# Kernel tuning notes

Measured on AMD Instinct MI355X. Metric: run time of the kernel, lower is better.

Reference implementation:

```python
import jax, jax.numpy as jnp
import numpy as np

GROUP_SIZE = 64
SHARED_EXPERT_WEIGHT = 1.0
# FP4 E2M1 codebook: sign bit + {0,.5,1,1.5,2,3,4,6}
FP4_TABLE = jnp.array([0.0, 0.5, 1.0, 1.5, 2.0, 3.0, 4.0, 6.0,
                       -0.0, -0.5, -1.0, -1.5, -2.0, -3.0, -4.0, -6.0], dtype=jnp.float32)


def dequant_fp4(packed, scales, group_size=GROUP_SIZE):
    """packed: [..., K//8, N] int32 (8 nibbles along K per word),
    scales: [..., K//group_size, N] -> dequantized [..., K, N] fp32."""
    shifts = (jnp.arange(8, dtype=jnp.int32) * 4)[:, None]          # [8,1]
    nib = jnp.right_shift(packed[..., :, None, :], shifts) & 0xF     # [..., K//8, 8, N]
    w = FP4_TABLE[nib]
    K = packed.shape[-2] * 8
    w = w.reshape(packed.shape[:-2] + (K, packed.shape[-1]))         # [..., K, N]
    s = jnp.repeat(scales, group_size, axis=-2)                      # [..., K, N]
    return w * s


def setup_inputs() -> dict:
    key = jax.random.key(0)
    ks = jax.random.split(key, 12)
    T, K, I, E, TOPK = 2048, 2048, 1024, 8, 2
    GS = GROUP_SIZE
    MAXI = 2**31 - 1
    u = lambda k, shp: jax.random.uniform(k, shp, jnp.float32, 0.005, 0.02)
    probs = jax.random.uniform(ks[10], (T, TOPK), jnp.float32)
    probs = probs / probs.sum(-1, keepdims=True)
    return {
        "hidden_states": jax.random.normal(ks[0], (T, K), jnp.float32),
        "gate_up_weight_packed": jax.random.randint(ks[1], (E, K // 8, 2 * I), 0, MAXI, jnp.int32),
        "gate_up_scales": u(ks[2], (E, K // GS, 2 * I)),
        "down_weight_packed": jax.random.randint(ks[3], (E, I // 8, K), 0, MAXI, jnp.int32),
        "down_scales": u(ks[4], (E, I // GS, K)),
        "shared_gate_up_packed": jax.random.randint(ks[5], (K // 8, 2 * I), 0, MAXI, jnp.int32),
        "shared_gate_up_scales": u(ks[6], (K // GS, 2 * I)),
        "shared_down_packed": jax.random.randint(ks[7], (I // 8, K), 0, MAXI, jnp.int32),
        "shared_down_scales": u(ks[8], (I // GS, K)),
        "expert_ids": jax.random.randint(ks[9], (T, TOPK), 0, E, jnp.int32),
        "expert_probs": probs,
    }


def reference(hidden_states, gate_up_weight_packed, gate_up_scales,
              down_weight_packed, down_scales,
              shared_gate_up_packed, shared_gate_up_scales,
              shared_down_packed, shared_down_scales,
              expert_ids, expert_probs):
    x = hidden_states                                                # [T, K]
    E = gate_up_weight_packed.shape[0]
    # --- routed experts: dequant + grouped GEMM over all tokens per expert ---
    Wgu = dequant_fp4(gate_up_weight_packed, gate_up_scales)         # [E, K, 2I]
    Wd = dequant_fp4(down_weight_packed, down_scales)                # [E, I, K]
    h = jnp.einsum('tk,ekn->etn', x, Wgu)                            # [E, T, 2I]
    gate, up = jnp.split(h, 2, axis=-1)
    act = jax.nn.silu(gate) * up                                     # [E, T, I]
    y = jnp.einsum('eti,eik->etk', act, Wd)                          # [E, T, K]
    # combine[t,e] = sum over top-k slots routed to e of prob
    one_hot = jax.nn.one_hot(expert_ids, E, dtype=x.dtype)           # [T, topk, E]
    combine = jnp.einsum('tk,tke->te', expert_probs, one_hot)        # [T, E]
    out = jnp.einsum('te,etk->tk', combine, y)                       # [T, K]
    # --- shared expert (always applied, weighted) ---
    Wgu_s = dequant_fp4(shared_gate_up_packed, shared_gate_up_scales)  # [K, 2I]
    Wd_s = dequant_fp4(shared_down_packed, shared_down_scales)         # [I, K]
    hs = x @ Wgu_s
    gs, us = jnp.split(hs, 2, axis=-1)
    shared_out = (jax.nn.silu(gs) * us) @ Wd_s
    return out + SHARED_EXPERT_WEIGHT * shared_out
```

## Files before the change

### kernel.cpp

```cpp
#include <hip/hip_runtime.h>
#include <hip/hip_bf16.h>

#define T_TOK 2048
#define K_DIM 2048
#define I_DIM 1024
#define NE    8
#define TOPK  2
#define GS    64

#define NSLOT  (T_TOK * TOPK)
#define TOTROW (NSLOT + T_TOK)
#define MAXITEM 32

typedef __attribute__((ext_vector_type(8))) short short8;
typedef __attribute__((ext_vector_type(4))) float f32x4;

#define WS_XB   ((size_t)65536)
#define WS_ACT  (WS_XB  + (size_t)2048 * 2048 * 2)
#define WS_Y    (WS_ACT + (size_t)TOTROW * 1024 * 2)


__device__ __forceinline__ unsigned pack2(float a, float b) {
    __hip_bfloat162 h = __float22bfloat162_rn(make_float2(a, b));
    return *reinterpret_cast<unsigned*>(&h);
}

__device__ __forceinline__ unsigned scale2(unsigned p, float s) {
    float f0 = __uint_as_float(p << 16) * s;
    float f1 = __uint_as_float(p & 0xFFFF0000u) * s;
    return pack2(f0, f1);
}

__device__ __forceinline__ float bf2f(ushort h) {
    return __uint_as_float((unsigned)h << 16);
}

__device__ __forceinline__ void dq_word(unsigned w, float s, unsigned o[4]) {
    unsigned lo  = w & 0x0F0F0F0Fu;
    unsigned hi  = (w >> 4) & 0x0F0F0F0Fu;
    unsigned mlo = lo & 0x07070707u, mhi = hi & 0x07070707u;
    unsigned Hlo = __builtin_amdgcn_perm(0x40404040u, 0x3F3F3F00u, mlo);
    unsigned Hhi = __builtin_amdgcn_perm(0x40404040u, 0x3F3F3F00u, mhi);
    unsigned Llo = __builtin_amdgcn_perm(0xC0804000u, 0xC0800000u, mlo);
    unsigned Lhi = __builtin_amdgcn_perm(0xC0804000u, 0xC0800000u, mhi);
    Hlo |= (lo & 0x08080808u) << 4;
    Hhi |= (hi & 0x08080808u) << 4;
    unsigned e01 = __builtin_amdgcn_perm(Hlo, Llo, 0x05010400u);
    unsigned e23 = __builtin_amdgcn_perm(Hlo, Llo, 0x07030602u);
    unsigned o01 = __builtin_amdgcn_perm(Hhi, Lhi, 0x05010400u);
    unsigned o23 = __builtin_amdgcn_perm(Hhi, Lhi, 0x07030602u);
    o[0] = scale2(e01, s); o[1] = scale2(e23, s);
    o[2] = scale2(o01, s); o[3] = scale2(o23, s);
}

__device__ __forceinline__ void gld16(const void* g, void* l) {
    __builtin_amdgcn_global_load_lds(
        (const __attribute__((address_space(1))) unsigned*)g,
        (__attribute__((address_space(3))) unsigned*)l, 16, 0, 0);
}

#define PREP_BLK 2048
#define FRONT_GRID (PREP_BLK + 1)

__global__ __launch_bounds__(256) void k_front(
        const float* __restrict__ x, ushort* __restrict__ xb,
        const int* __restrict__ eids,
        int* __restrict__ gcnt, int* __restrict__ gbase,
        int* __restrict__ tileCnt, int* __restrict__ tileE, int* __restrict__ tileM,
        int* __restrict__ tok, int* __restrict__ inv) {
    int id = blockIdx.x;
    int tid = threadIdx.x;

    if (id < PREP_BLK) {
        int idx = id * 256 + tid;
        const float4* p = (const float4*)(x + (size_t)idx * 8);
        float4 f0 = p[0], f1 = p[1];
        unsigned u0 = pack2(f0.x, f0.z);
        unsigned u1 = pack2(f1.x, f1.z);
        unsigned u2 = pack2(f0.y, f0.w);
        unsigned u3 = pack2(f1.y, f1.w);
        *(int4*)(xb + (size_t)idx * 8) = make_int4(u0, u1, u2, u3);
    } else {
        __shared__ int lcnt[NE], lbase[NE], lcur[NE];
        if (tid < NE) lcnt[tid] = 0;
        __syncthreads();
        for (int i = tid; i < NSLOT; i += 256)
            atomicAdd(&lcnt[eids[i]], 1);
        __syncthreads();
        if (tid == 0) {
            int acc = 0;
            for (int e = 0; e < NE; e++) { lbase[e] = acc; acc += lcnt[e]; }
        }
        __syncthreads();
        if (tid < NE) lcur[tid] = lbase[tid];
        __syncthreads();
        for (int i = tid; i < NSLOT; i += 256) {
            int e = eids[i];
            int pos = atomicAdd(&lcur[e], 1);
            tok[pos] = i >> 1;
            inv[i] = pos;
        }
        for (int t = tid; t < T_TOK; t += 256)
            tok[NSLOT + t] = t;
        if (tid < NE) { gcnt[tid] = lcnt[tid]; gbase[tid] = lbase[tid]; }
        if (tid == 0) {
            gcnt[NE] = T_TOK; gbase[NE] = NSLOT;
            int nt = 0;
            for (int e = 0; e < NE + 1; e++) {
                int c = (e < NE) ? lcnt[e] : T_TOK;
                for (int m = 0; m < c; m += 256) { tileE[nt] = e; tileM[nt] = m; nt++; }
            }
            *tileCnt = nt;
            for (int i = nt; i < 64; i++) { tileE[i] = 0; tileM[i] = 0; }
        }
    }
}

__global__ __launch_bounds__(512) void k_gemm_gateup(
        const ushort* __restrict__ xb,
        const int* __restrict__ gup, const float* __restrict__ gus,
        const int* __restrict__ sup, const float* __restrict__ sus,
        const int* __restrict__ gcnt, const int* __restrict__ gbase,
        const int* __restrict__ tileCnt, const int* __restrict__ tileE,
        const int* __restrict__ tileM,
        const int* __restrict__ tokid, ushort* __restrict__ act) {
    int item = blockIdx.y;
    if (item >= *tileCnt) return;
    int tid = threadIdx.x;
    int e = tileE[item], m0 = tileM[item];
    int cnt = gcnt[e], base = gbase[e];
    int n0 = blockIdx.x * 64;
    const int* wp; const float* sc;
    if (e < NE) { wp = gup + (size_t)e * 256 * 2048; sc = gus + (size_t)e * 32 * 2048; }
    else        { wp = sup; sc = sus; }

    __shared__ __align__(16) ushort xs[2][256 * 64];
    __shared__ __align__(16) ushort bs[128 * 64];

    int lane = tid & 63, wv = tid >> 6;
    int lid = lane & 15, quad = lane >> 4;
    int wr = wv >> 1, wc = wv & 1;
    int l8 = lane >> 3, l7 = lane & 7;
    int chunk = (l7 ^ l8) * 8;

    const ushort* aSrc[4];
    #pragma unroll
    for (int it = 0; it < 4; it++) {
        int rA = wv * 32 + it * 8 + l8;
        int t = (m0 + rA < cnt) ? tokid[base + m0 + rA] : 0;
        aSrc[it] = xb + (size_t)t * K_DIM + chunk;
    }

    int nloc = tid & 127;
    int kw0 = (tid >> 7) * 2;
    int bj = nloc & 63, bh = nloc >> 6;
    int ncol = (bj < 32) ? (n0 + bh * 32 + bj) : (I_DIM + n0 + bh * 32 + (bj - 32));
    int bd0 = nloc * 64 + ((kw0    ) ^ (nloc & 7)) * 8;
    int bd1 = nloc * 64 + ((kw0 + 1) ^ (nloc & 7)) * 8;

    const int NT = K_DIM / 64;
    const int* wq = wp + (size_t)kw0 * 2048 + ncol;
    const float* sq = sc + ncol;

    #pragma unroll
    for (int it = 0; it < 4; it++) {
        gld16(aSrc[it], &xs[0][(wv * 4 + it) * 512]);
        aSrc[it] += 64;
    }
    unsigned w0 = (unsigned)wq[0];
    unsigned w1 = (unsigned)wq[2048];
    float s = *sq;
    wq += 16384; sq += 2048;

    f32x4 acc[4][4] = {};
    int pp = 0;

    for (int t = 0; t < NT; ++t) {
        __syncthreads();
        {
            unsigned o[4];
            dq_word(w0, s, o); *(int4*)&bs[bd0] = make_int4(o[0], o[1], o[2], o[3]);
            dq_word(w1, s, o); *(int4*)&bs[bd1] = make_int4(o[0], o[1], o[2], o[3]);
        }
        __syncthreads();
        if (t + 1 < NT) {
            #pragma unroll
            for (int it = 0; it < 4; it++) {
                gld16(aSrc[it], &xs[pp ^ 1][(wv * 4 + it) * 512]);
                aSrc[it] += 64;
            }
            w0 = (unsigned)wq[0];
            w1 = (unsigned)wq[2048];
            s = *sq;
            wq += 16384; sq += 2048;
        }
        __builtin_amdgcn_sched_barrier(0);
        __builtin_amdgcn_s_setprio(1);
        #pragma unroll
        for (int ks = 0; ks < 2; ks++) {
            int slot = ((ks * 4 + quad) ^ l7) * 8;
            short8 a[4], b[4];
            #pragma unroll
            for (int mt = 0; mt < 4; mt++)
                a[mt] = *(const short8*)&xs[pp][(wr * 64 + mt * 16 + lid) * 64 + slot];
            #pragma unroll
            for (int nt = 0; nt < 4; nt++)
                b[nt] = *(const short8*)&bs[(wc * 64 + nt * 16 + lid) * 64 + slot];
            #pragma unroll
            for (int mt = 0; mt < 4; mt++)
                #pragma unroll
                for (int nt = 0; nt < 4; nt++)
                    acc[mt][nt] = __builtin_amdgcn_mfma_f32_16x16x32_bf16(
                        a[mt], b[nt], acc[mt][nt], 0, 0, 0);
        }
        __builtin_amdgcn_s_setprio(0);
        pp ^= 1;
    }

    int c7 = lid & 7;
    int delta = ((c7 >> 1) + ((c7 & 1) << 2)) - c7;
    #pragma unroll
    for (int mt = 0; mt < 4; mt++) {
        #pragma unroll
        for (int i = 0; i < 4; i++) {
            int row = wr * 64 + mt * 16 + quad * 4 + i;
            if (m0 + row < cnt) {
                size_t p = (size_t)(base + m0 + row);
                #pragma unroll
                for (int nt = 0; nt < 2; nt++) {
                    float g = acc[mt][nt][i], u = acc[mt][nt + 2][i];
                    float vv = g / (1.f + __expf(-g)) * u;
                    int ncol2 = n0 + wc * 32 + nt * 16 + lid;
                    __hip_bfloat16 hb = __float2bfloat16(vv);
                    act[p * I_DIM + ncol2 + delta] = *reinterpret_cast<ushort*>(&hb);
                }
            }
        }
    }
}

__global__ __launch_bounds__(512) void k_gemm_down(
        const ushort* __restrict__ actb,
        const int* __restrict__ dwp, const float* __restrict__ dsc,
        const int* __restrict__ sdp, const float* __restrict__ sds,
        const int* __restrict__ gcnt, const int* __restrict__ gbase,
        const int* __restrict__ tileCnt, const int* __restrict__ tileE,
        const int* __restrict__ tileM,
        ushort* __restrict__ y) {
    int item = blockIdx.y;
    if (item >= *tileCnt) return;
    int tid = threadIdx.x;
    int e = tileE[item], m0 = tileM[item];
    int cnt = gcnt[e], base = gbase[e];
    int n0 = blockIdx.x * 128;
    const int* wp; const float* sc;
    if (e < NE) { wp = dwp + (size_t)e * 128 * 2048; sc = dsc + (size_t)e * 16 * 2048; }
    else        { wp = sdp; sc = sds; }

    __shared__ __align__(16) ushort xs[2][256 * 64];
    __shared__ __align__(16) ushort bs[128 * 64];

    int lane = tid & 63, wv = tid >> 6;
    int lid = lane & 15, quad = lane >> 4;
    int wr = wv >> 1, wc = wv & 1;
    int l8 = lane >> 3, l7 = lane & 7;
    int chunk = (l7 ^ l8) * 8;

    const ushort* aSrc[4];
    #pragma unroll
    for (int it = 0; it < 4; it++) {
        int rA = wv * 32 + it * 8 + l8;
        int rr = m0 + rA; if (rr >= cnt) rr = cnt - 1;
        aSrc[it] = actb + (size_t)(base + rr) * I_DIM + chunk;
    }

    int nloc = tid & 127;
    int kw0 = (tid >> 7) * 2;
    int ncol = n0 + nloc;
    int bd0 = nloc * 64 + ((kw0    ) ^ (nloc & 7)) * 8;
    int bd1 = nloc * 64 + ((kw0 + 1) ^ (nloc & 7)) * 8;

    const int NT = I_DIM / 64;
    const int* wq = wp + (size_t)kw0 * 2048 + ncol;
    const float* sq = sc + ncol;

    #pragma unroll
    for (int it = 0; it < 4; it++) {
        gld16(aSrc[it], &xs[0][(wv * 4 + it) * 512]);
        aSrc[it] += 64;
    }
    unsigned w0 = (unsigned)wq[0];
    unsigned w1 = (unsigned)wq[2048];
    float s = *sq;
    wq += 16384; sq += 2048;

    f32x4 acc[4][4] = {};
    int pp = 0;

    for (int t = 0; t < NT; ++t) {
        __syncthreads();
        {
            unsigned o[4];
            dq_word(w0, s, o); *(int4*)&bs[bd0] = make_int4(o[0], o[1], o[2], o[3]);
            dq_word(w1, s, o); *(int4*)&bs[bd1] = make_int4(o[0], o[1], o[2], o[3]);
        }
        __syncthreads();
        if (t + 1 < NT) {
            #pragma unroll
            for (int it = 0; it < 4; it++) {
                gld16(aSrc[it], &xs[pp ^ 1][(wv * 4 + it) * 512]);
                aSrc[it] += 64;
            }
            w0 = (unsigned)wq[0];
            w1 = (unsigned)wq[2048];
            s = *sq;
            wq += 16384; sq += 2048;
        }
        __builtin_amdgcn_sched_barrier(0);
        __builtin_amdgcn_s_setprio(1);
        #pragma unroll
        for (int ks = 0; ks < 2; ks++) {
            int slot = ((ks * 4 + quad) ^ l7) * 8;
            short8 a[4], b[4];
            #pragma unroll
            for (int mt = 0; mt < 4; mt++)
                a[mt] = *(const short8*)&xs[pp][(wr * 64 + mt * 16 + lid) * 64 + slot];
            #pragma unroll
            for (int nt = 0; nt < 4; nt++)
                b[nt] = *(const short8*)&bs[(wc * 64 + nt * 16 + lid) * 64 + slot];
            #pragma unroll
            for (int mt = 0; mt < 4; mt++)
                #pragma unroll
                for (int nt = 0; nt < 4; nt++)
                    acc[mt][nt] = __builtin_amdgcn_mfma_f32_16x16x32_bf16(
                        a[mt], b[nt], acc[mt][nt], 0, 0, 0);
        }
        __builtin_amdgcn_s_setprio(0);
        pp ^= 1;
    }

    #pragma unroll
    for (int mt = 0; mt < 4; mt++) {
        #pragma unroll
        for (int i = 0; i < 4; i++) {
            int row = wr * 64 + mt * 16 + quad * 4 + i;
            if (m0 + row < cnt) {
                ushort* yrow = y + (size_t)(base + m0 + row) * 2048 + n0 + wc * 64 + lid;
                #pragma unroll
                for (int nt = 0; nt < 4; nt++) {
                    __hip_bfloat16 hb = __float2bfloat16(acc[mt][nt][i]);
                    yrow[nt * 16] = *reinterpret_cast<ushort*>(&hb);
                }
            }
        }
    }
}

__global__ __launch_bounds__(256) void k_combine(
        const ushort* __restrict__ y, const int* __restrict__ inv,
        const float* __restrict__ prb, float* __restrict__ out) {
    int idx = blockIdx.x * 256 + threadIdx.x;
    int t = idx >> 8;
    int c = (idx & 255) * 8;
    int p0 = inv[2 * t], p1 = inv[2 * t + 1];
    float w0 = prb[2 * t], w1 = prb[2 * t + 1];
    int4 a = *(const int4*)(y + (size_t)p0 * 2048 + c);
    int4 b = *(const int4*)(y + (size_t)p1 * 2048 + c);
    int4 s = *(const int4*)(y + (size_t)(NSLOT + t) * 2048 + c);
    const ushort* au = (const ushort*)&a;
    const ushort* bu = (const ushort*)&b;
    const ushort* su = (const ushort*)&s;
    float o[8];
    #pragma unroll
    for (int j = 0; j < 8; j++)
        o[j] = w0 * bf2f(au[j]) + w1 * bf2f(bu[j]) + bf2f(su[j]);
    *(float4*)(out + (size_t)t * 2048 + c)     = *(float4*)&o[0];
    *(float4*)(out + (size_t)t * 2048 + c + 4) = *(float4*)&o[4];
}

extern "C" void kernel_launch(void* const* d_in, const int* in_sizes, int n_in,
                              void* d_out, int out_size, void* d_ws, size_t ws_size,
                              hipStream_t stream) {
    const float* x    = (const float*)d_in[0];
    const int*   gup  = (const int*)d_in[1];
    const float* gus  = (const float*)d_in[2];
    const int*   dwp  = (const int*)d_in[3];
    const float* dsc  = (const float*)d_in[4];
    const int*   sup  = (const int*)d_in[5];
    const float* sus  = (const float*)d_in[6];
    const int*   sdp  = (const int*)d_in[7];
    const float* sds  = (const float*)d_in[8];
    const int*   eids = (const int*)d_in[9];
    const float* prb  = (const float*)d_in[10];
    float* out = (float*)d_out;

    char*   ws      = (char*)d_ws;
    int*    gcnt    = (int*)(ws + 0);
    int*    gbase   = (int*)(ws + 64);
    int*    tileCnt = (int*)(ws + 128);
    int*    tileE   = (int*)(ws + 192);
    int*    tileM   = (int*)(ws + 448);
    int*    tok     = (int*)(ws + 1024);
    int*    inv     = (int*)(ws + 25600);
    ushort* xb      = (ushort*)(ws + WS_XB);
    ushort* act     = (ushort*)(ws + WS_ACT);
    ushort* y       = (ushort*)(ws + WS_Y);

    k_front<<<FRONT_GRID, 256, 0, stream>>>(
        x, xb, eids, gcnt, gbase, tileCnt, tileE, tileM, tok, inv);
    k_gemm_gateup<<<dim3(I_DIM / 64, MAXITEM), 512, 0, stream>>>(
        xb, gup, gus, sup, sus, gcnt, gbase, tileCnt, tileE, tileM, tok, act);
    k_gemm_down<<<dim3(K_DIM / 128, MAXITEM), 512, 0, stream>>>(
        act, dwp, dsc, sdp, sds, gcnt, gbase, tileCnt, tileE, tileM, y);
    k_combine<<<(T_TOK * K_DIM / 8) / 256, 256, 0, stream>>>(y, inv, prb, out);
}
```

Baseline: 234.2 us.

## Double-buffer dequantized weights and widen GEMM tiles with interleaved phase pipeline

Both grouped GEMMs move to 256x256 output tiles (8 waves as 2x4), so each block covers twice as many N columns, and the dequantized B tile gets double-buffered in LDS. The K loop is split into four MFMA phases. Between phases the code interleaves the next A-tile async loads, the dequantization of the next B sub-slice and weight prefetch two steps ahead, using explicit s_barrier and waitcnt control. The aim is to hide the global-load and dequant latency behind MFMA and to raise the per-block reuse of A. The cost is more LDS (about 128KB), twice the accumulator registers, fewer blocks in the grid, and fragile hand-tuned waitcnt ordering.

```diff
diff --git a/kernel.cpp b/kernel.cpp
--- a/kernel.cpp
+++ b/kernel.cpp
@@ -116,7 +116,7 @@
     }
 }
 
-__global__ __launch_bounds__(512) void k_gemm_gateup(
+__global__ __launch_bounds__(512, 2) void k_gemm_gateup(
         const ushort* __restrict__ xb,
         const int* __restrict__ gup, const float* __restrict__ gus,
         const int* __restrict__ sup, const float* __restrict__ sus,
@@ -129,17 +129,17 @@
     int tid = threadIdx.x;
     int e = tileE[item], m0 = tileM[item];
     int cnt = gcnt[e], base = gbase[e];
-    int n0 = blockIdx.x * 64;
+    int n0 = blockIdx.x * 128;
     const int* wp; const float* sc;
     if (e < NE) { wp = gup + (size_t)e * 256 * 2048; sc = gus + (size_t)e * 32 * 2048; }
     else        { wp = sup; sc = sus; }
 
     __shared__ __align__(16) ushort xs[2][256 * 64];
-    __shared__ __align__(16) ushort bs[128 * 64];
+    __shared__ __align__(16) ushort bs[2][256 * 64];
 
     int lane = tid & 63, wv = tid >> 6;
     int lid = lane & 15, quad = lane >> 4;
-    int wr = wv >> 1, wc = wv & 1;
+    int wr = wv >> 2, wc = wv & 3;
     int l8 = lane >> 3, l7 = lane & 7;
     int chunk = (l7 ^ l8) * 8;
 
@@ -151,95 +151,176 @@
         aSrc[it] = xb + (size_t)t * K_DIM + chunk;
     }
 
-    int nloc = tid & 127;
-    int kw0 = (tid >> 7) * 2;
-    int bj = nloc & 63, bh = nloc >> 6;
-    int ncol = (bj < 32) ? (n0 + bh * 32 + bj) : (I_DIM + n0 + bh * 32 + (bj - 32));
-    int bd0 = nloc * 64 + ((kw0    ) ^ (nloc & 7)) * 8;
-    int bd1 = nloc * 64 + ((kw0 + 1) ^ (nloc & 7)) * 8;
+    int col = tid & 255;
+    int kw0 = (tid >> 8) * 4;
+    int jj = col & 63, wq_ = col >> 6;
+    int ncol = (jj < 32) ? (n0 + wq_ * 32 + jj) : (I_DIM + n0 + wq_ * 32 + (jj - 32));
+    int bd0 = col * 64 + ((kw0    ) ^ (col & 7)) * 8;
+    int bd1 = col * 64 + ((kw0 + 1) ^ (col & 7)) * 8;
+    int bd2 = col * 64 + ((kw0 + 2) ^ (col & 7)) * 8;
+    int bd3 = col * 64 + ((kw0 + 3) ^ (col & 7)) * 8;
 
     const int NT = K_DIM / 64;
-    const int* wq = wp + (size_t)kw0 * 2048 + ncol;
-    const float* sq = sc + ncol;
 
     #pragma unroll
     for (int it = 0; it < 4; it++) {
         gld16(aSrc[it], &xs[0][(wv * 4 + it) * 512]);
         aSrc[it] += 64;
     }
-    unsigned w0 = (unsigned)wq[0];
-    unsigned w1 = (unsigned)wq[2048];
-    float s = *sq;
-    wq += 16384; sq += 2048;
-
-    f32x4 acc[4][4] = {};
-    int pp = 0;
-
+    {
+        float s0 = sc[ncol];
+        unsigned o[4];
+        unsigned w;
+        w = (unsigned)wp[(size_t)(kw0    ) * 2048 + ncol];
+        dq_word(w, s0, o); *(int4*)&bs[0][bd0] = make_int4(o[0], o[1], o[2], o[3]);
+        w = (unsigned)wp[(size_t)(kw0 + 1) * 2048 + ncol];
+        dq_word(w, s0, o); *(int4*)&bs[0][bd1] = make_int4(o[0], o[1], o[2], o[3]);
+        w = (unsigned)wp[(size_t)(kw0 + 2) * 2048 + ncol];
+        dq_word(w, s0, o); *(int4*)&bs[0][bd2] = make_int4(o[0], o[1], o[2], o[3]);
+        w = (unsigned)wp[(size_t)(kw0 + 3) * 2048 + ncol];
+        dq_word(w, s0, o); *(int4*)&bs[0][bd3] = make_int4(o[0], o[1], o[2], o[3]);
+    }
+    unsigned wd0 = (unsigned)wp[(size_t)(8 + kw0    ) * 2048 + ncol];
+    unsigned wd1 = (unsigned)wp[(size_t)(8 + kw0 + 1) * 2048 + ncol];
+    unsigned wd2 = (unsigned)wp[(size_t)(8 + kw0 + 2) * 2048 + ncol];
+    unsigned wd3 = (unsigned)wp[(size_t)(8 + kw0 + 3) * 2048 + ncol];
+    float sd = sc[2048 + ncol];
+    __syncthreads();
+
+    f32x4 acc[8][4] = {};
+
+    #pragma unroll 1
     for (int t = 0; t < NT; ++t) {
-        __syncthreads();
-        {
-            unsigned o[4];
-            dq_word(w0, s, o); *(int4*)&bs[bd0] = make_int4(o[0], o[1], o[2], o[3]);
-            dq_word(w1, s, o); *(int4*)&bs[bd1] = make_int4(o[0], o[1], o[2], o[3]);
-        }
-        __syncthreads();
-        if (t + 1 < NT) {
-            #pragma unroll
-            for (int it = 0; it < 4; it++) {
-                gld16(aSrc[it], &xs[pp ^ 1][(wv * 4 + it) * 512]);
-                aSrc[it] += 64;
-            }
-            w0 = (unsigned)wq[0];
-            w1 = (unsigned)wq[2048];
-            s = *sq;
-            wq += 16384; sq += 2048;
-        }
-        __builtin_amdgcn_sched_barrier(0);
-        __builtin_amdgcn_s_setprio(1);
-        #pragma unroll
-        for (int ks = 0; ks < 2; ks++) {
-            int slot = ((ks * 4 + quad) ^ l7) * 8;
-            short8 a[4], b[4];
-            #pragma unroll
-            for (int mt = 0; mt < 4; mt++)
-                a[mt] = *(const short8*)&xs[pp][(wr * 64 + mt * 16 + lid) * 64 + slot];
-            #pragma unroll
-            for (int nt = 0; nt < 4; nt++)
-                b[nt] = *(const short8*)&bs[(wc * 64 + nt * 16 + lid) * 64 + slot];
-            #pragma unroll
-            for (int mt = 0; mt < 4; mt++)
-                #pragma unroll
-                for (int nt = 0; nt < 4; nt++)
-                    acc[mt][nt] = __builtin_amdgcn_mfma_f32_16x16x32_bf16(
-                        a[mt], b[nt], acc[mt][nt], 0, 0, 0);
-        }
-        __builtin_amdgcn_s_setprio(0);
-        pp ^= 1;
+        int p = t & 1, q = p ^ 1;
+        int t2 = (t + 2 < NT) ? (t + 2) : (NT - 1);
+        const int* wlp = wp + (size_t)(t2 * 8 + kw0) * 2048 + ncol;
+        unsigned wl0, wl1, wl2, wl3; float sl;
+        short8 a[4], b[4];
+        unsigned o[4];
+
+        {
+            int slot = (quad ^ l7) * 8;
+            #pragma unroll
+            for (int mt = 0; mt < 4; mt++)
+                a[mt] = *(const short8*)&xs[p][(wr * 128 + mt * 16 + lid) * 64 + slot];
+            #pragma unroll
+            for (int nt = 0; nt < 4; nt++)
+                b[nt] = *(const short8*)&bs[p][(wc * 64 + nt * 16 + lid) * 64 + slot];
+        }
+        gld16(aSrc[0], &xs[q][(wv * 4 + 0) * 512]); aSrc[0] += 64;
+        gld16(aSrc[1], &xs[q][(wv * 4 + 1) * 512]); aSrc[1] += 64;
+        dq_word(wd0, sd, o); *(int4*)&bs[q][bd0] = make_int4(o[0], o[1], o[2], o[3]);
+        __builtin_amdgcn_s_barrier();
+        asm volatile("s_waitcnt lgkmcnt(0)" ::: "memory");
+        __builtin_amdgcn_sched_barrier(0);
+        __builtin_amdgcn_s_setprio(1);
+        #pragma unroll
+        for (int mt = 0; mt < 4; mt++)
+            #pragma unroll
+            for (int nt = 0; nt < 4; nt++)
+                acc[mt][nt] = __builtin_amdgcn_mfma_f32_16x16x32_bf16(
+                    a[mt], b[nt], acc[mt][nt], 0, 0, 0);
+        __builtin_amdgcn_s_setprio(0);
+        __builtin_amdgcn_s_barrier();
+
+        {
+            int slot = (quad ^ l7) * 8;
+            #pragma unroll
+            for (int mt = 0; mt < 4; mt++)
+                a[mt] = *(const short8*)&xs[p][(wr * 128 + 64 + mt * 16 + lid) * 64 + slot];
+        }
+        gld16(aSrc[2], &xs[q][(wv * 4 + 2) * 512]); aSrc[2] += 64;
+        gld16(aSrc[3], &xs[q][(wv * 4 + 3) * 512]); aSrc[3] += 64;
+        dq_word(wd1, sd, o); *(int4*)&bs[q][bd1] = make_int4(o[0], o[1], o[2], o[3]);
+        __builtin_amdgcn_s_barrier();
+        asm volatile("s_waitcnt lgkmcnt(0)" ::: "memory");
+        __builtin_amdgcn_sched_barrier(0);
+        __builtin_amdgcn_s_setprio(1);
+        #pragma unroll
+        for (int mt = 0; mt < 4; mt++)
+            #pragma unroll
+            for (int nt = 0; nt < 4; nt++)
+                acc[4 + mt][nt] = __builtin_amdgcn_mfma_f32_16x16x32_bf16(
+                    a[mt], b[nt], acc[4 + mt][nt], 0, 0, 0);
+        __builtin_amdgcn_s_setprio(0);
+        __builtin_amdgcn_s_barrier();
+
+        {
+            int slot = ((4 + quad) ^ l7) * 8;
+            #pragma unroll
+            for (int mt = 0; mt < 4; mt++)
+                a[mt] = *(const short8*)&xs[p][(wr * 128 + mt * 16 + lid) * 64 + slot];
+            #pragma unroll
+            for (int nt = 0; nt < 4; nt++)
+                b[nt] = *(const short8*)&bs[p][(wc * 64 + nt * 16 + lid) * 64 + slot];
+        }
+        wl0 = (unsigned)wlp[0];
+        wl1 = (unsigned)wlp[2048];
+        dq_word(wd2, sd, o); *(int4*)&bs[q][bd2] = make_int4(o[0], o[1], o[2], o[3]);
+        __builtin_amdgcn_s_barrier();
+        asm volatile("s_waitcnt lgkmcnt(0)" ::: "memory");
+        __builtin_amdgcn_sched_barrier(0);
+        __builtin_amdgcn_s_setprio(1);
+        #pragma unroll
+        for (int mt = 0; mt < 4; mt++)
+            #pragma unroll
+            for (int nt = 0; nt < 4; nt++)
+                acc[mt][nt] = __builtin_amdgcn_mfma_f32_16x16x32_bf16(
+                    a[mt], b[nt], acc[mt][nt], 0, 0, 0);
+        __builtin_amdgcn_s_setprio(0);
+        __builtin_amdgcn_s_barrier();
+
+        {
+            int slot = ((4 + quad) ^ l7) * 8;
+            #pragma unroll
+            for (int mt = 0; mt < 4; mt++)
+                a[mt] = *(const short8*)&xs[p][(wr * 128 + 64 + mt * 16 + lid) * 64 + slot];
+        }
+        wl2 = (unsigned)wlp[4096];
+        wl3 = (unsigned)wlp[6144];
+        sl  = sc[(size_t)t2 * 2048 + ncol];
+        dq_word(wd3, sd, o); *(int4*)&bs[q][bd3] = make_int4(o[0], o[1], o[2], o[3]);
+        __builtin_amdgcn_s_barrier();
+        asm volatile("s_waitcnt lgkmcnt(0)" ::: "memory");
+        __builtin_amdgcn_sched_barrier(0);
+        __builtin_amdgcn_s_setprio(1);
+        #pragma unroll
+        for (int mt = 0; mt < 4; mt++)
+            #pragma unroll
+            for (int nt = 0; nt < 4; nt++)
+                acc[4 + mt][nt] = __builtin_amdgcn_mfma_f32_16x16x32_bf16(
+                    a[mt], b[nt], acc[4 + mt][nt], 0, 0, 0);
+        __builtin_amdgcn_s_setprio(0);
+        asm volatile("s_waitcnt vmcnt(5)" ::: "memory");
+        __builtin_amdgcn_s_barrier();
+        __builtin_amdgcn_sched_barrier(0);
+
+        wd0 = wl0; wd1 = wl1; wd2 = wl2; wd3 = wl3; sd = sl;
     }
 
     int c7 = lid & 7;
     int delta = ((c7 >> 1) + ((c7 & 1) << 2)) - c7;
     #pragma unroll
-    for (int mt = 0; mt < 4; mt++) {
+    for (int am = 0; am < 8; am++) {
         #pragma unroll
         for (int i = 0; i < 4; i++) {
-            int row = wr * 64 + mt * 16 + quad * 4 + i;
+            int row = wr * 128 + am * 16 + quad * 4 + i;
             if (m0 + row < cnt) {
-                size_t p = (size_t)(base + m0 + row);
+                size_t pr = (size_t)(base + m0 + row);
                 #pragma unroll
                 for (int nt = 0; nt < 2; nt++) {
-                    float g = acc[mt][nt][i], u = acc[mt][nt + 2][i];
+                    float g = acc[am][nt][i], u = acc[am][nt + 2][i];
                     float vv = g / (1.f + __expf(-g)) * u;
                     int ncol2 = n0 + wc * 32 + nt * 16 + lid;
                     __hip_bfloat16 hb = __float2bfloat16(vv);
-                    act[p * I_DIM + ncol2 + delta] = *reinterpret_cast<ushort*>(&hb);
+                    act[pr * I_DIM + ncol2 + delta] = *reinterpret_cast<ushort*>(&hb);
                 }
             }
         }
     }
 }
 
-__global__ __launch_bounds__(512) void k_gemm_down(
+__global__ __launch_bounds__(512, 2) void k_gemm_down(
         const ushort* __restrict__ actb,
         const int* __restrict__ dwp, const float* __restrict__ dsc,
         const int* __restrict__ sdp, const float* __restrict__ sds,
@@ -252,17 +333,17 @@
     int tid = threadIdx.x;
     int e = tileE[item], m0 = tileM[item];
     int cnt = gcnt[e], base = gbase[e];
-    int n0 = blockIdx.x * 128;
+    int n0 = blockIdx.x * 256;
     const int* wp; const float* sc;
     if (e < NE) { wp = dwp + (size_t)e * 128 * 2048; sc = dsc + (size_t)e * 16 * 2048; }
     else        { wp = sdp; sc = sds; }
 
     __shared__ __align__(16) ushort xs[2][256 * 64];
-    __shared__ __align__(16) ushort bs[128 * 64];
+    __shared__ __align__(16) ushort bs[2][256 * 64];
 
     int lane = tid & 63, wv = tid >> 6;
     int lid = lane & 15, quad = lane >> 4;
-    int wr = wv >> 1, wc = wv & 1;
+    int wr = wv >> 2, wc = wv & 3;
     int l8 = lane >> 3, l7 = lane & 7;
     int chunk = (l7 ^ l8) * 8;
 
@@ -274,81 +355,162 @@
         aSrc[it] = actb + (size_t)(base + rr) * I_DIM + chunk;
     }
 
-    int nloc = tid & 127;
-    int kw0 = (tid >> 7) * 2;
-    int ncol = n0 + nloc;
-    int bd0 = nloc * 64 + ((kw0    ) ^ (nloc & 7)) * 8;
-    int bd1 = nloc * 64 + ((kw0 + 1) ^ (nloc & 7)) * 8;
+    int col = tid & 255;
+    int kw0 = (tid >> 8) * 4;
+    int ncol = n0 + col;
+    int bd0 = col * 64 + ((kw0    ) ^ (col & 7)) * 8;
+    int bd1 = col * 64 + ((kw0 + 1) ^ (col & 7)) * 8;
+    int bd2 = col * 64 + ((kw0 + 2) ^ (col & 7)) * 8;
+    int bd3 = col * 64 + ((kw0 + 3) ^ (col & 7)) * 8;
 
     const int NT = I_DIM / 64;
-    const int* wq = wp + (size_t)kw0 * 2048 + ncol;
-    const float* sq = sc + ncol;
 
     #pragma unroll
     for (int it = 0; it < 4; it++) {
         gld16(aSrc[it], &xs[0][(wv * 4 + it) * 512]);
         aSrc[it] += 64;
     }
-    unsigned w0 = (unsigned)wq[0];
-    unsigned w1 = (unsigned)wq[2048];
-    float s = *sq;
-    wq += 16384; sq += 2048;
-
-    f32x4 acc[4][4] = {};
-    int pp = 0;
-
+    {
+        float s0 = sc[ncol];
+        unsigned o[4];
+        unsigned w;
+        w = (unsigned)wp[(size_t)(kw0    ) * 2048 + ncol];
+        dq_word(w, s0, o); *(int4*)&bs[0][bd0] = make_int4(o[0], o[1], o[2], o[3]);
+        w = (unsigned)wp[(size_t)(kw0 + 1) * 2048 + ncol];
+        dq_word(w, s0, o); *(int4*)&bs[0][bd1] = make_int4(o[0], o[1], o[2], o[3]);
+        w = (unsigned)wp[(size_t)(kw0 + 2) * 2048 + ncol];
+        dq_word(w, s0, o); *(int4*)&bs[0][bd2] = make_int4(o[0], o[1], o[2], o[3]);
+        w = (unsigned)wp[(size_t)(kw0 + 3) * 2048 + ncol];
+        dq_word(w, s0, o); *(int4*)&bs[0][bd3] = make_int4(o[0], o[1], o[2], o[3]);
+    }
+    unsigned wd0 = (unsigned)wp[(size_t)(8 + kw0    ) * 2048 + ncol];
+    unsigned wd1 = (unsigned)wp[(size_t)(8 + kw0 + 1) * 2048 + ncol];
+    unsigned wd2 = (unsigned)wp[(size_t)(8 + kw0 + 2) * 2048 + ncol];
+    unsigned wd3 = (unsigned)wp[(size_t)(8 + kw0 + 3) * 2048 + ncol];
+    float sd = sc[2048 + ncol];
+    __syncthreads();
+
+    f32x4 acc[8][4] = {};
+
+    #pragma unroll 1
     for (int t = 0; t < NT; ++t) {
-        __syncthreads();
-        {
-            unsigned o[4];
-            dq_word(w0, s, o); *(int4*)&bs[bd0] = make_int4(o[0], o[1], o[2], o[3]);
-            dq_word(w1, s, o); *(int4*)&bs[bd1] = make_int4(o[0], o[1], o[2], o[3]);
-        }
-        __syncthreads();
-        if (t + 1 < NT) {
-            #pragma unroll
-            for (int it = 0; it < 4; it++) {
-                gld16(aSrc[it], &xs[pp ^ 1][(wv * 4 + it) * 512]);
-                aSrc[it] += 64;
-            }
-            w0 = (unsigned)wq[0];
-            w1 = (unsigned)wq[2048];
-            s = *sq;
-            wq += 16384; sq += 2048;
-        }
-        __builtin_amdgcn_sched_barrier(0);
-        __builtin_amdgcn_s_setprio(1);
-        #pragma unroll
-        for (int ks = 0; ks < 2; ks++) {
-            int slot = ((ks * 4 + quad) ^ l7) * 8;
-            short8 a[4], b[4];
-            #pragma unroll
-            for (int mt = 0; mt < 4; mt++)
-                a[mt] = *(const short8*)&xs[pp][(wr * 64 + mt * 16 + lid) * 64 + slot];
-            #pragma unroll
-            for (int nt = 0; nt < 4; nt++)
-                b[nt] = *(const short8*)&bs[(wc * 64 + nt * 16 + lid) * 64 + slot];
-            #pragma unroll
-            for (int mt = 0; mt < 4; mt++)
-                #pragma unroll
-                for (int nt = 0; nt < 4; nt++)
-                    acc[mt][nt] = __builtin_amdgcn_mfma_f32_16x16x32_bf16(
-                        a[mt], b[nt], acc[mt][nt], 0, 0, 0);
-        }
-        __builtin_amdgcn_s_setprio(0);
-        pp ^= 1;
-    }
-
-    #pragma unroll
-    for (int mt = 0; mt < 4; mt++) {
+        int p = t & 1, q = p ^ 1;
+        int t2 = (t + 2 < NT) ? (t + 2) : (NT - 1);
+        const int* wlp = wp + (size_t)(t2 * 8 + kw0) * 2048 + ncol;
+        unsigned wl0, wl1, wl2, wl3; float sl;
+        short8 a[4], b[4];
+        unsigned o[4];
+
+        {
+            int slot = (quad ^ l7) * 8;
+            #pragma unroll
+            for (int mt = 0; mt < 4; mt++)
+                a[mt] = *(const short8*)&xs[p][(wr * 128 + mt * 16 + lid) * 64 + slot];
+            #pragma unroll
+            for (int nt = 0; nt < 4; nt++)
+                b[nt] = *(const short8*)&bs[p][(wc * 64 + nt * 16 + lid) * 64 + slot];
+        }
+        gld16(aSrc[0], &xs[q][(wv * 4 + 0) * 512]); aSrc[0] += 64;
+        gld16(aSrc[1], &xs[q][(wv * 4 + 1) * 512]); aSrc[1] += 64;
+        dq_word(wd0, sd, o); *(int4*)&bs[q][bd0] = make_int4(o[0], o[1], o[2], o[3]);
+        __builtin_amdgcn_s_barrier();
+        asm volatile("s_waitcnt lgkmcnt(0)" ::: "memory");
+        __builtin_amdgcn_sched_barrier(0);
+        __builtin_amdgcn_s_setprio(1);
+        #pragma unroll
+        for (int mt = 0; mt < 4; mt++)
+            #pragma unroll
+            for (int nt = 0; nt < 4; nt++)
+                acc[mt][nt] = __builtin_amdgcn_mfma_f32_16x16x32_bf16(
+                    a[mt], b[nt], acc[mt][nt], 0, 0, 0);
+        __builtin_amdgcn_s_setprio(0);
+        __builtin_amdgcn_s_barrier();
+
+        {
+            int slot = (quad ^ l7) * 8;
+            #pragma unroll
+            for (int mt = 0; mt < 4; mt++)
+                a[mt] = *(const short8*)&xs[p][(wr * 128 + 64 + mt * 16 + lid) * 64 + slot];
+        }
+        gld16(aSrc[2], &xs[q][(wv * 4 + 2) * 512]); aSrc[2] += 64;
+        gld16(aSrc[3], &xs[q][(wv * 4 + 3) * 512]); aSrc[3] += 64;
+        dq_word(wd1, sd, o); *(int4*)&bs[q][bd1] = make_int4(o[0], o[1], o[2], o[3]);
+        __builtin_amdgcn_s_barrier();
+        asm volatile("s_waitcnt lgkmcnt(0)" ::: "memory");
+        __builtin_amdgcn_sched_barrier(0);
+        __builtin_amdgcn_s_setprio(1);
+        #pragma unroll
+        for (int mt = 0; mt < 4; mt++)
+            #pragma unroll
+            for (int nt = 0; nt < 4; nt++)
+                acc[4 + mt][nt] = __builtin_amdgcn_mfma_f32_16x16x32_bf16(
+                    a[mt], b[nt], acc[4 + mt][nt], 0, 0, 0);
+        __builtin_amdgcn_s_setprio(0);
+        __builtin_amdgcn_s_barrier();
+
+        {
+            int slot = ((4 + quad) ^ l7) * 8;
+            #pragma unroll
+            for (int mt = 0; mt < 4; mt++)
+                a[mt] = *(const short8*)&xs[p][(wr * 128 + mt * 16 + lid) * 64 + slot];
+            #pragma unroll
+            for (int nt = 0; nt < 4; nt++)
+                b[nt] = *(const short8*)&bs[p][(wc * 64 + nt * 16 + lid) * 64 + slot];
+        }
+        wl0 = (unsigned)wlp[0];
+        wl1 = (unsigned)wlp[2048];
+        dq_word(wd2, sd, o); *(int4*)&bs[q][bd2] = make_int4(o[0], o[1], o[2], o[3]);
+        __builtin_amdgcn_s_barrier();
+        asm volatile("s_waitcnt lgkmcnt(0)" ::: "memory");
+        __builtin_amdgcn_sched_barrier(0);
+        __builtin_amdgcn_s_setprio(1);
+        #pragma unroll
+        for (int mt = 0; mt < 4; mt++)
+            #pragma unroll
+            for (int nt = 0; nt < 4; nt++)
+                acc[mt][nt] = __builtin_amdgcn_mfma_f32_16x16x32_bf16(
+                    a[mt], b[nt], acc[mt][nt], 0, 0, 0);
+        __builtin_amdgcn_s_setprio(0);
+        __builtin_amdgcn_s_barrier();
+
+        {
+            int slot = ((4 + quad) ^ l7) * 8;
+            #pragma unroll
+            for (int mt = 0; mt < 4; mt++)
+                a[mt] = *(const short8*)&xs[p][(wr * 128 + 64 + mt * 16 + lid) * 64 + slot];
+        }
+        wl2 = (unsigned)wlp[4096];
+        wl3 = (unsigned)wlp[6144];
+        sl  = sc[(size_t)t2 * 2048 + ncol];
+        dq_word(wd3, sd, o); *(int4*)&bs[q][bd3] = make_int4(o[0], o[1], o[2], o[3]);
+        __builtin_amdgcn_s_barrier();
+        asm volatile("s_waitcnt lgkmcnt(0)" ::: "memory");
+        __builtin_amdgcn_sched_barrier(0);
+        __builtin_amdgcn_s_setprio(1);
+        #pragma unroll
+        for (int mt = 0; mt < 4; mt++)
+            #pragma unroll
+            for (int nt = 0; nt < 4; nt++)
+                acc[4 + mt][nt] = __builtin_amdgcn_mfma_f32_16x16x32_bf16(
+                    a[mt], b[nt], acc[4 + mt][nt], 0, 0, 0);
+        __builtin_amdgcn_s_setprio(0);
+        asm volatile("s_waitcnt vmcnt(5)" ::: "memory");
+        __builtin_amdgcn_s_barrier();
+        __builtin_amdgcn_sched_barrier(0);
+
+        wd0 = wl0; wd1 = wl1; wd2 = wl2; wd3 = wl3; sd = sl;
+    }
+
+    #pragma unroll
+    for (int am = 0; am < 8; am++) {
         #pragma unroll
         for (int i = 0; i < 4; i++) {
-            int row = wr * 64 + mt * 16 + quad * 4 + i;
+            int row = wr * 128 + am * 16 + quad * 4 + i;
             if (m0 + row < cnt) {
                 ushort* yrow = y + (size_t)(base + m0 + row) * 2048 + n0 + wc * 64 + lid;
                 #pragma unroll
                 for (int nt = 0; nt < 4; nt++) {
-                    __hip_bfloat16 hb = __float2bfloat16(acc[mt][nt][i]);
+                    __hip_bfloat16 hb = __float2bfloat16(acc[am][nt][i]);
                     yrow[nt * 16] = *reinterpret_cast<ushort*>(&hb);
                 }
             }
@@ -408,9 +570,9 @@
 
     k_front<<<FRONT_GRID, 256, 0, stream>>>(
         x, xb, eids, gcnt, gbase, tileCnt, tileE, tileM, tok, inv);
-    k_gemm_gateup<<<dim3(I_DIM / 64, MAXITEM), 512, 0, stream>>>(
+    k_gemm_gateup<<<dim3(I_DIM / 128, MAXITEM), 512, 0, stream>>>(
         xb, gup, gus, sup, sus, gcnt, gbase, tileCnt, tileE, tileM, tok, act);
-    k_gemm_down<<<dim3(K_DIM / 128, MAXITEM), 512, 0, stream>>>(
+    k_gemm_down<<<dim3(K_DIM / 256, MAXITEM), 512, 0, stream>>>(
         act, dwp, dsc, sdp, sds, gcnt, gbase, tileCnt, tileE, tileM, y);
     k_combine<<<(T_TOK * K_DIM / 8) / 256, 256, 0, stream>>>(y, inv, prb, out);
 }
```

Result: slower. 255.7 us (+9.2%).
